# Performance work log

Measured on AMD Instinct MI355X. Metric: run time of the kernel, lower is better.

The kernel has to match this reference:

```python
import jax, jax.numpy as jnp
import numpy as np

T, B, D_IN = 1024, 64, 17
H_MAIN = 150   # per-direction hidden of main bi-GRU (hidden_dim=300)
H_HIER = 128   # per-direction hidden of hier bi-GRU (hier_hidden=256)
M = 16         # uniform measure length (eoM fires every M steps)
N_MEAS = T // M
N_PITCH, N_KS = 35, 15
PAD_P, PAD_K = 34, 14


def _gru(x, Wih, Whh, bih, bhh):
    # x: [T, N, D]; torch GRU gate order is (r, z, n)
    H = Whh.shape[1]
    gi_all = jnp.einsum('tnd,gd->tng', x, Wih) + bih  # input-side gates, precomputed

    def step(h, gi):
        gh = h @ Whh.T + bhh
        ir, iz, inn = jnp.split(gi, 3, axis=-1)
        hr, hz, hn = jnp.split(gh, 3, axis=-1)
        r = jax.nn.sigmoid(ir + hr)
        z = jax.nn.sigmoid(iz + hz)
        n = jnp.tanh(inn + r * hn)
        h_new = (1.0 - z) * n + z * h
        return h_new, h_new

    h0 = jnp.zeros((x.shape[1], H), x.dtype)
    _, ys = jax.lax.scan(step, h0, gi_all)
    return ys


def _bigru(x, pf, pb):
    yf = _gru(x, *pf)
    yb = _gru(x[::-1], *pb)[::-1]
    return jnp.concatenate([yf, yb], axis=-1)


def _ce(logits, targets, pad_idx):
    # mean cross-entropy with ignore_index=pad_idx
    logp = jax.nn.log_softmax(logits, axis=-1)
    mask = (targets != pad_idx).astype(logits.dtype)
    nll = -jnp.take_along_axis(logp, targets[:, None], axis=1)[:, 0]
    return jnp.sum(nll * mask) / jnp.maximum(jnp.sum(mask), 1.0)


def _forward(sentences, mWih_f, mWhh_f, mbih_f, mbhh_f, mWih_b, mWhh_b, mbih_b, mbhh_b,
             hWih_f, hWhh_f, hbih_f, hbhh_f, hWih_b, hWhh_b, hbih_b, hbhh_b,
             Wq, bq, Wv, bv, Wp, bp, Wk, bk, pitches, keysignatures):
    # main bi-GRU over full sequences: [T, B, 300]
    rnn_out = _bigru(sentences, (mWih_f, mWhh_f, mbih_f, mbhh_f),
                     (mWih_b, mWhh_b, mbih_b, mbhh_b))
    H2 = rnn_out.shape[-1]
    # carve uniform measures: [T,B,H2] -> [M, B*N_MEAS, H2]
    seg = rnn_out.reshape(N_MEAS, M, B, H2).transpose(1, 2, 0, 3).reshape(M, B * N_MEAS, H2)
    hier = _bigru(seg, (hWih_f, hWhh_f, hbih_f, hbhh_f),
                  (hWih_b, hWhh_b, hbih_b, hbhh_b))  # [M, B*N_MEAS, 256]
    HH = hier.shape[-1]
    # attention per measure: query = value = hier outputs [B*N_MEAS, M, 256]
    hv = hier.reshape(M, B, N_MEAS, HH).transpose(1, 2, 0, 3).reshape(B * N_MEAS, M, HH)
    q = hv @ Wq.T + bq
    v = hv @ Wv.T + bv
    attn = jax.nn.softmax(jnp.einsum('nld,nmd->nlm', q, v), axis=-1)
    ctx = jnp.einsum('nlm,nmd->nd', attn, hv).reshape(B, N_MEAS, HH)  # sum over l of attn@value
    # repeat each measure context over its M timesteps: [T, B, 256]
    ctx_t = jnp.repeat(ctx, M, axis=1).transpose(1, 0, 2)
    stacked = jnp.concatenate([rnn_out, ctx_t], axis=-1)  # [T, B, 556]
    out_pitch = stacked @ Wp.T + bp   # [T, B, 35]
    out_ks = ctx_t @ Wk.T + bk        # [T, B, 15]
    return (_ce(out_pitch.reshape(-1, N_PITCH), pitches.reshape(-1), PAD_P)
            + _ce(out_ks.reshape(-1, N_KS), keysignatures.reshape(-1), PAD_K))


def setup_inputs() -> dict:
    key = jax.random.key(0)
    ks = jax.random.split(key, 32)

    def w(i, *shape):
        return jax.random.normal(ks[i], shape, jnp.float32) * 0.05

    G_M, G_H = 3 * H_MAIN, 3 * H_HIER
    inp = {
        'sentences': jax.random.normal(ks[0], (T, B, D_IN), jnp.float32),
        'pitches': jax.random.randint(ks[1], (T, B), 0, PAD_P),
        'keysignatures': jax.random.randint(ks[2], (T, B), 0, PAD_K),
        'sentences_len': jnp.full((B,), T, dtype=jnp.int32),
        'eoM': jnp.tile(((jnp.arange(T) % M) == M - 1).astype(jnp.int32)[:, None], (1, B)),
        'mWih_f': w(3, G_M, D_IN), 'mWhh_f': w(4, G_M, H_MAIN), 'mbih_f': w(5, G_M), 'mbhh_f': w(6, G_M),
        'mWih_b': w(7, G_M, D_IN), 'mWhh_b': w(8, G_M, H_MAIN), 'mbih_b': w(9, G_M), 'mbhh_b': w(10, G_M),
        'hWih_f': w(11, G_H, 2 * H_MAIN), 'hWhh_f': w(12, G_H, H_HIER), 'hbih_f': w(13, G_H), 'hbhh_f': w(14, G_H),
        'hWih_b': w(15, G_H, 2 * H_MAIN), 'hWhh_b': w(16, G_H, H_HIER), 'hbih_b': w(17, G_H), 'hbhh_b': w(18, G_H),
        'Wq': w(19, 2 * H_HIER, 2 * H_HIER), 'bq': w(20, 2 * H_HIER),
        'Wv': w(21, 2 * H_HIER, 2 * H_HIER), 'bv': w(22, 2 * H_HIER),
        'Wp': w(23, N_PITCH, 2 * H_MAIN + 2 * H_HIER), 'bp': w(24, N_PITCH),
        'Wk': w(25, N_KS, 2 * H_HIER), 'bk': w(26, N_KS),
    }
    return inp


def reference(sentences, pitches, keysignatures, sentences_len, eoM,
              mWih_f, mWhh_f, mbih_f, mbhh_f, mWih_b, mWhh_b, mbih_b, mbhh_b,
              hWih_f, hWhh_f, hbih_f, hbhh_f, hWih_b, hWhh_b, hbih_b, hbhh_b,
              Wq, bq, Wv, bv, Wp, bp, Wk, bk):
    # sentences_len/eoM encode the (uniform) measure structure M=16, full lengths;
    # the segment layout is baked in statically, so they are structural constants here.
    return _forward(sentences, mWih_f, mWhh_f, mbih_f, mbhh_f, mWih_b, mWhh_b, mbih_b, mbhh_b,
                    hWih_f, hWhh_f, hbih_f, hbhh_f, hWih_b, hWhh_b, hbih_b, hbhh_b,
                    Wq, bq, Wv, bv, Wp, bp, Wk, bk, pitches, keysignatures)
```

## Files before the change

### kernel.cpp

```cpp
#include <hip/hip_runtime.h>
#include <cstddef>

constexpr int kT   = 1024;
constexpr int kB   = 64;
constexpr int kDIN = 17;
constexpr int kHM  = 150;
constexpr int kHH  = 128;
constexpr int kM   = 16;
constexpr int kD2  = 300;
constexpr int kNP  = 35;
constexpr int kNK  = 15;

constexpr size_t OFF_RNN16  = 0;
constexpr size_t OFF_HV16   = 10485760;
constexpr size_t OFF_CTX    = 18874368;
constexpr size_t OFF_PT     = 19922944;
constexpr size_t OFF_PTPACK = 19988480;
constexpr size_t OFF_U      = 20021248;
constexpr size_t OFF_W      = 20021504;
constexpr size_t OFF_C0     = 20021760;
constexpr size_t OFF_ACC    = 20021776;
constexpr size_t OFF_KSLOGP = 20021792;
constexpr size_t OFF_CLOG   = 20083232;
constexpr size_t OFF_BPACKM = 20226592;
constexpr size_t OFF_BPACK  = 20318752;
constexpr size_t OFF_BPACKL = 20490784;

typedef __bf16 bf16x8 __attribute__((ext_vector_type(8)));
typedef float f32x4 __attribute__((ext_vector_type(4)));

__device__ __forceinline__ unsigned short f2bf(float f) {
  unsigned u = __float_as_uint(f);
  u += 0x7FFFu + ((u >> 16) & 1u);
  return (unsigned short)(u >> 16);
}
__device__ __forceinline__ float bf2f(unsigned short v) {
  return __uint_as_float(((unsigned)v) << 16);
}
__device__ __forceinline__ float sigm(float x) {
  return __builtin_amdgcn_rcpf(1.f + __expf(-x));
}
__device__ __forceinline__ float tanh_fast(float x) {
  return 1.f - 2.f * __builtin_amdgcn_rcpf(__expf(2.f * x) + 1.f);
}

__global__ void k_pt(const float* __restrict__ Wq, const float* __restrict__ Wv,
                     float* __restrict__ PT) {
  const int e = blockIdx.x, c = threadIdx.x;
  float acc = 0.f;
  for (int a = 0; a < 256; a++) acc += Wq[a * 256 + c] * Wv[a * 256 + e];
  PT[e * 256 + c] = acc;
}

__global__ void k_ptsmall(const float* __restrict__ PT,
                          const float* __restrict__ Wq, const float* __restrict__ bq,
                          const float* __restrict__ Wv, const float* __restrict__ bv,
                          unsigned short* __restrict__ pp,
                          float* __restrict__ u, float* __restrict__ w,
                          float* __restrict__ c0, float* __restrict__ acc) {
  const int bid = blockIdx.x;
  if (bid < 128) {
    if (threadIdx.x >= 64) return;
    const int kt = bid & 7, nt = bid >> 3;
    const int lane = threadIdx.x;
    const int c = nt * 16 + (lane & 15);
    const int e0 = kt * 32 + (lane >> 4) * 8;
#pragma unroll
    for (int j = 0; j < 8; j++)
      pp[((size_t)bid * 64 + lane) * 8 + j] = f2bf(PT[(e0 + j) * 256 + c]);
  } else {
    const int a = threadIdx.x;
    float us = 0.f, ws = 0.f;
    for (int j = 0; j < 256; j++) {
      us += Wq[j * 256 + a] * bv[j];
      ws += bq[j] * Wv[j * 256 + a];
    }
    u[a] = us; w[a] = ws;
    if (a == 0) {
      float c = 0.f;
      for (int j = 0; j < 256; j++) c += bq[j] * bv[j];
      c0[0] = c;
      acc[0] = acc[1] = acc[2] = acc[3] = 0.f;
    }
  }
}

__global__ void k_repack_all(
    const float* __restrict__ mWih_f, const float* __restrict__ mWhh_f,
    const float* __restrict__ mWih_b, const float* __restrict__ mWhh_b,
    const float* __restrict__ hWih_f, const float* __restrict__ hWhh_f,
    const float* __restrict__ hWih_b, const float* __restrict__ hWhh_b,
    const float* __restrict__ Wp,
    unsigned short* __restrict__ bpackM, unsigned short* __restrict__ bpack,
    unsigned short* __restrict__ bpackL) {
  const int lane = threadIdx.x;
  int bid = blockIdx.x;
  if (bid < 360) {
    const int kt = bid % 6;
    const int gt = (bid / 6) % 30;
    const int d  = bid / 180;
    const float* Wih = d ? mWih_b : mWih_f;
    const float* Whh = d ? mWhh_b : mWhh_f;
    const int slot = gt * 16 + (lane & 15);
    const int type = slot / 160, j = slot - type * 160;
    const int row = type * 150 + j;
    const bool valid = (j < 150);
    const int kbase = (lane >> 4) * 8;
    unsigned short* dst = bpackM + ((((size_t)d * 30 + gt) * 6 + kt) * 64 + lane) * 8;
#pragma unroll
    for (int jj = 0; jj < 8; jj++) {
      float f = 0.f;
      if (valid) {
        if (kt < 5) {
          const int k = kt * 32 + kbase + jj;
          if (k < 150) f = Whh[row * 150 + k];
        } else {
          const int k = kbase + jj;
          if (k < 17) f = Wih[row * 17 + k];
        }
      }
      dst[jj] = f2bf(f);
    }
  } else if (bid < 1032) {
    bid -= 360;
    const int kt = bid % 14;
    const int nt = (bid / 14) % 24;
    const int d  = bid / (14 * 24);
    const float* Wih = d ? hWih_b : hWih_f;
    const float* Whh = d ? hWhh_b : hWhh_f;
    const int n = nt * 16 + (lane & 15);
    const int kbase = kt * 32 + (lane >> 4) * 8;
    unsigned short* dst = bpack + ((((size_t)d * 24 + nt) * 14 + kt) * 64 + lane) * 8;
#pragma unroll
    for (int j = 0; j < 8; j++) {
      const int k = kbase + j;
      float f = 0.f;
      if (kt < 10) {
        if (k < 150) f = Wih[n * 300 + k];
        else if (k >= 160 && k < 310) f = Wih[n * 300 + (k - 10)];
      } else {
        f = Whh[n * 128 + (k - 320)];
      }
      dst[j] = f2bf(f);
    }
  } else {
    bid -= 1032;
    const int kt = bid % 10, nt = bid / 10;
    const int n = nt * 16 + (lane & 15);
    const int kbase = kt * 32 + (lane >> 4) * 8;
    unsigned short* dst = bpackL + (((size_t)bid) * 64 + lane) * 8;
#pragma unroll
    for (int j = 0; j < 8; j++) {
      const int k = kbase + j;
      float f = 0.f;
      if (n < kNP) {
        if (k < 150) f = Wp[n * 556 + k];
        else if (k >= 160 && k < 310) f = Wp[n * 556 + (k - 10)];
      }
      dst[j] = f2bf(f);
    }
  }
}

__global__ __launch_bounds__(640, 2) void k_main_gru_mfma(
    const float* __restrict__ x,
    const unsigned short* __restrict__ bpackM,
    const float* __restrict__ bihf, const float* __restrict__ bhhf,
    const float* __restrict__ bihb, const float* __restrict__ bhhb,
    unsigned short* __restrict__ rnn16)
{
  const int d = blockIdx.x & 1, b = blockIdx.x >> 1;
  const int tid = threadIdx.x, w = tid >> 6, lane = tid & 63;
  const int col = lane & 15, q8 = (lane >> 4) * 8;
  __shared__ __align__(16) unsigned short hx[2][160];
  __shared__ __align__(16) unsigned short hist[2][16][160];
  __shared__ __align__(16) unsigned short xall[kT][32];
  for (int i = tid; i < 2 * 160; i += 640) ((unsigned short*)hx)[i] = 0;
  for (int i = tid; i < 2 * 16 * 160; i += 640) ((unsigned short*)hist)[i] = 0;
  for (int i = tid; i < kT * 32; i += 640) {
    const int t = i >> 5, c = i & 31;
    xall[t][c] = (c < kDIN) ? f2bf(x[((size_t)t * kB + b) * kDIN + c]) : (unsigned short)0;
  }
  const float* bih = d ? bihb : bihf;
  const float* bhh = d ? bhhb : bhhf;
  const int j = w * 16 + col;
  const bool actv = (lane < 16) && (j < kHM);
  float br = 0.f, bz = 0.f, bnx = 0.f, bnh = 0.f;
  if (actv) {
    br  = bih[j] + bhh[j];
    bz  = bih[150 + j] + bhh[150 + j];
    bnx = bih[300 + j];
    bnh = bhh[300 + j];
  }
  bf16x8 bw[3][6];
  const unsigned short* bp = bpackM + (size_t)d * 30 * 6 * 64 * 8;
  const int gts[3] = { w, 10 + w, 20 + w };
#pragma unroll
  for (int gi = 0; gi < 3; gi++)
#pragma unroll
    for (int kt = 0; kt < 6; kt++)
      bw[gi][kt] = *(const bf16x8*)&bp[(((size_t)gts[gi] * 6 + kt) * 64 + lane) * 8];
  float h_old = 0.f;
  __syncthreads();

  for (int t = 0; t < kT; t++) {
    const int tx = d ? (kT - 1 - t) : t;
    const int buf = t & 1;
    bf16x8 afr[6];
#pragma unroll
    for (int kt = 0; kt < 5; kt++) afr[kt] = *(const bf16x8*)&hx[buf][kt * 32 + q8];
    afr[5] = *(const bf16x8*)&xall[tx][q8];
    f32x4 aR0 = (f32x4)(0.f), aR1 = (f32x4)(0.f);
    f32x4 aZ0 = (f32x4)(0.f), aZ1 = (f32x4)(0.f);
    f32x4 aN0 = (f32x4)(0.f), aN1 = (f32x4)(0.f);
    f32x4 aX  = (f32x4)(0.f);
#pragma unroll
    for (int kt = 0; kt < 6; kt++) {
      const bf16x8 af = afr[kt];
      if ((kt & 1) == 0) {
        aR0 = __builtin_amdgcn_mfma_f32_16x16x32_bf16(af, bw[0][kt], aR0, 0, 0, 0);
        aZ0 = __builtin_amdgcn_mfma_f32_16x16x32_bf16(af, bw[1][kt], aZ0, 0, 0, 0);
        aN0 = __builtin_amdgcn_mfma_f32_16x16x32_bf16(af, bw[2][kt], aN0, 0, 0, 0);
      } else if (kt < 5) {
        aR1 = __builtin_amdgcn_mfma_f32_16x16x32_bf16(af, bw[0][kt], aR1, 0, 0, 0);
        aZ1 = __builtin_amdgcn_mfma_f32_16x16x32_bf16(af, bw[1][kt], aZ1, 0, 0, 0);
        aN1 = __builtin_amdgcn_mfma_f32_16x16x32_bf16(af, bw[2][kt], aN1, 0, 0, 0);
      } else {
        aR1 = __builtin_amdgcn_mfma_f32_16x16x32_bf16(af, bw[0][5], aR1, 0, 0, 0);
        aZ1 = __builtin_amdgcn_mfma_f32_16x16x32_bf16(af, bw[1][5], aZ1, 0, 0, 0);
        aX  = __builtin_amdgcn_mfma_f32_16x16x32_bf16(af, bw[2][5], aX, 0, 0, 0);
      }
    }
    if (actv) {
      const float r = sigm(aR0[0] + aR1[0] + br);
      const float z = sigm(aZ0[0] + aZ1[0] + bz);
      const float n = tanh_fast(aX[0] + bnx + r * (aN0[0] + aN1[0] + bnh));
      h_old = (1.f - z) * n + z * h_old;
      const unsigned short us = f2bf(h_old);
      hx[buf ^ 1][j] = us;
      hist[(t >> 4) & 1][t & 15][j] = us;
    }
    __syncthreads();
    if ((t & 15) == 15) {
      const int hb = (t >> 4) & 1;
      const int toff = tid / 40, ch = tid - toff * 40;
      const int tg = t - 15 + toff;
      const int txg = d ? (kT - 1 - tg) : tg;
      *(ushort4*)&rnn16[((size_t)txg * kB + b) * 320 + d * 160 + ch * 4] =
          *(const ushort4*)&hist[hb][toff][ch * 4];
    }
  }
}

__global__ __launch_bounds__(512, 1) void k_hier_mfma(
    const unsigned short* __restrict__ rnn16,
    const unsigned short* __restrict__ bpack,
    const float* __restrict__ bihf, const float* __restrict__ bhhf,
    const float* __restrict__ bihb, const float* __restrict__ bhhb,
    unsigned short* __restrict__ hv16)
{
  const int d = blockIdx.x & 1;
  const int bn0 = (blockIdx.x >> 1) * 16;
  const int tid = threadIdx.x;
  const int w = tid >> 6;
  const int lane = tid & 63;
  const int q = lane >> 4, col = lane & 15, q8 = q * 8;

  __shared__ __align__(16) unsigned short x_s[2][16][328];
  __shared__ __align__(16) unsigned short h_s[16][136];

  for (int i = tid; i < 16 * 136; i += 512) ((unsigned short*)h_s)[i] = 0;
  const float* bih = d ? bihb : bihf;
  const float* bhh = d ? bhhb : bhhf;
  const int j = w * 16 + col;
  const float biR  = bih[j] + bhh[j];
  const float biZ  = bih[128 + j] + bhh[128 + j];
  const float biNX = bih[256 + j];
  const float biNH = bhh[256 + j];
  float h32r[4] = {0.f, 0.f, 0.f, 0.f};

  bf16x8 bw[3][14];
  const unsigned short* bpd = bpack + (size_t)d * 24 * 14 * 64 * 8;
  const int nts[3] = { w, 8 + w, 16 + w };
#pragma unroll
  for (int gi = 0; gi < 3; gi++)
#pragma unroll
    for (int kt = 0; kt < 14; kt++)
      bw[gi][kt] = *(const bf16x8*)&bpd[(((size_t)nts[gi] * 14 + kt) * 64 + lane) * 8];

  {
    const int mx0 = d ? 15 : 0;
    for (int i = tid; i < 640; i += 512) {
      const int r = i / 40, c = i - r * 40;
      const int bn = bn0 + r, bb = bn >> 6, nn = bn & 63;
      *(uint4*)&x_s[0][r][c * 8] =
          *(const uint4*)&rnn16[((size_t)(nn * 16 + mx0) * 64 + bb) * 320 + c * 8];
    }
  }
  __syncthreads();

  for (int m = 0; m < kM; m++) {
    const int mx = d ? (15 - m) : m;
    const int buf = m & 1;
    f32x4 aR = (f32x4)(0.f), aZ = (f32x4)(0.f), aNX = (f32x4)(0.f), aNH = (f32x4)(0.f);
#pragma unroll
    for (int kt = 0; kt < 14; kt++) {
      const bf16x8 af = (kt < 10) ? *(const bf16x8*)&x_s[buf][col][kt * 32 + q8]
                                  : *(const bf16x8*)&h_s[col][(kt - 10) * 32 + q8];
      aR = __builtin_amdgcn_mfma_f32_16x16x32_bf16(af, bw[0][kt], aR, 0, 0, 0);
      aZ = __builtin_amdgcn_mfma_f32_16x16x32_bf16(af, bw[1][kt], aZ, 0, 0, 0);
      if (kt < 10) aNX = __builtin_amdgcn_mfma_f32_16x16x32_bf16(af, bw[2][kt], aNX, 0, 0, 0);
      else         aNH = __builtin_amdgcn_mfma_f32_16x16x32_bf16(af, bw[2][kt], aNH, 0, 0, 0);
    }
    __syncthreads();
#pragma unroll
    for (int i = 0; i < 4; i++) {
      const int row = q * 4 + i;
      const float rr = sigm(aR[i] + biR);
      const float zz = sigm(aZ[i] + biZ);
      const float nn2 = tanh_fast(aNX[i] + biNX + rr * (aNH[i] + biNH));
      const float hnew = (1.f - zz) * nn2 + zz * h32r[i];
      h32r[i] = hnew;
      const unsigned short us = f2bf(hnew);
      h_s[row][j] = us;
      hv16[((size_t)(bn0 + row) * kM + mx) * 256 + d * kHH + j] = us;
    }
    if (m + 1 < kM) {
      const int mxn = d ? (15 - (m + 1)) : (m + 1);
      for (int i = tid; i < 640; i += 512) {
        const int r = i / 40, c = i - r * 40;
        const int bn = bn0 + r, bb = bn >> 6, nn = bn & 63;
        *(uint4*)&x_s[buf ^ 1][r][c * 8] =
            *(const uint4*)&rnn16[((size_t)(nn * 16 + mxn) * 64 + bb) * 320 + c * 8];
      }
    }
    __syncthreads();
  }
}

__global__ __launch_bounds__(256) void k_attn2(
    const unsigned short* __restrict__ hv16, const unsigned short* __restrict__ ptpack,
    const float* __restrict__ u, const float* __restrict__ w,
    const float* __restrict__ c0p, float* __restrict__ ctx) {
  const int tid = threadIdx.x;
  const int wv = tid >> 6, lane = tid & 63, col = lane & 15, q = lane >> 4, q8 = q * 8;
  __shared__ __align__(16) unsigned short hv16s[16][264];
  __shared__ __align__(16) unsigned short Ts16[16][264];
  __shared__ float pu[16][17], pw[16][17];
  __shared__ float uh[16], wh[16], SM[16];
  __shared__ float As[16][17];
  const float c0 = c0p[0];
  bf16x8 bpt[4][8];
#pragma unroll
  for (int i2 = 0; i2 < 4; i2++)
#pragma unroll
    for (int kt = 0; kt < 8; kt++)
      bpt[i2][kt] = *(const bf16x8*)&ptpack[((((size_t)(wv * 4 + i2)) * 8 + kt) * 64 + lane) * 8];

  for (int ni = 0; ni < 4; ni++) {
    const int n = blockIdx.x * 4 + ni;
    {
      const unsigned short* src = hv16 + (size_t)n * 4096;
      const int row = tid >> 4, ci = (tid & 15) * 16;
#pragma unroll
      for (int k = 0; k < 16; k += 4)
        *(ushort4*)&hv16s[row][ci + k] = *(const ushort4*)&src[row * 256 + ci + k];
    }
    __syncthreads();
    {
      f32x4 acc[4];
#pragma unroll
      for (int i2 = 0; i2 < 4; i2++) acc[i2] = (f32x4)(0.f);
#pragma unroll
      for (int kt = 0; kt < 8; kt++) {
        const bf16x8 af = *(const bf16x8*)&hv16s[col][kt * 32 + q8];
#pragma unroll
        for (int i2 = 0; i2 < 4; i2++)
          acc[i2] = __builtin_amdgcn_mfma_f32_16x16x32_bf16(af, bpt[i2][kt], acc[i2], 0, 0, 0);
      }
#pragma unroll
      for (int i2 = 0; i2 < 4; i2++) {
        const int nt = wv * 4 + i2;
#pragma unroll
        for (int i = 0; i < 4; i++) Ts16[q * 4 + i][nt * 16 + col] = f2bf(acc[i2][i]);
      }
    }
    {
      const int l = tid >> 4, s = tid & 15;
      float su = 0.f, sw = 0.f;
#pragma unroll
      for (int a0 = 0; a0 < 16; a0++) {
        const int a = s * 16 + a0;
        const float hvv = bf2f(hv16s[l][a]);
        su += hvv * u[a];
        sw += hvv * w[a];
      }
      pu[l][s] = su; pw[l][s] = sw;
    }
    __syncthreads();
    if (tid < 16) { float s2 = 0.f; for (int s = 0; s < 16; s++) s2 += pu[tid][s]; uh[tid] = s2; }
    else if (tid < 32) { float s2 = 0.f; for (int s = 0; s < 16; s++) s2 += pw[tid - 16][s]; wh[tid - 16] = s2; }
    __syncthreads();
    if (tid < 64) {
      f32x4 sa = (f32x4)(0.f);
#pragma unroll
      for (int kt = 0; kt < 8; kt++) {
        const bf16x8 af  = *(const bf16x8*)&hv16s[col][kt * 32 + q8];
        const bf16x8 bts = *(const bf16x8*)&Ts16[col][kt * 32 + q8];
        sa = __builtin_amdgcn_mfma_f32_16x16x32_bf16(af, bts, sa, 0, 0, 0);
      }
#pragma unroll
      for (int i = 0; i < 4; i++) {
        const int l = q * 4 + i;
        float sc = sa[i] + c0 + uh[l] + wh[col];
        float mxv = sc;
#pragma unroll
        for (int o = 8; o >= 1; o >>= 1) mxv = fmaxf(mxv, __shfl_xor(mxv, o, 16));
        const float e = __expf(sc - mxv);
        float se = e;
#pragma unroll
        for (int o = 8; o >= 1; o >>= 1) se += __shfl_xor(se, o, 16);
        As[l][col] = e / se;
      }
    }
    __syncthreads();
    if (tid < 16) {
      float s = 0.f;
      for (int l2 = 0; l2 < 16; l2++) s += As[l2][tid];
      SM[tid] = s;
    }
    __syncthreads();
    float cv = 0.f;
#pragma unroll
    for (int m2 = 0; m2 < 16; m2++) cv += SM[m2] * bf2f(hv16s[m2][tid]);
    ctx[(size_t)n * 256 + tid] = cv;
    __syncthreads();
  }
}

__global__ __launch_bounds__(256) void k_ctxlog2(
    const float* __restrict__ ctx, const float* __restrict__ Wp, const float* __restrict__ bp,
    const float* __restrict__ Wk, const float* __restrict__ bk,
    float* __restrict__ clog, float* __restrict__ kslogp) {
  const int tid = threadIdx.x;
  __shared__ __align__(16) float W2[50][260];
  __shared__ __align__(16) float cs[256];
  __shared__ float arr[64];
  __shared__ float bps[35], bks[15];
  for (int i = tid; i < 35 * 256; i += 256) { const int r = i >> 8, c = i & 255; W2[r][c] = Wp[r * 556 + 300 + c]; }
  for (int i = tid; i < 15 * 256; i += 256) { const int r = i >> 8, c = i & 255; W2[35 + r][c] = Wk[r * 256 + c]; }
  if (tid < 35) bps[tid] = bp[tid];
  else if (tid < 50) bks[tid - 35] = bk[tid - 35];
  __syncthreads();
  const int o = tid >> 2, s = tid & 3;
  for (int it = 0; it < 16; it++) {
    const int bn = blockIdx.x * 16 + it;
    cs[tid] = ctx[(size_t)bn * 256 + tid];
    __syncthreads();
    float v = 0.f;
    if (o < 50) {
      for (int k0 = 0; k0 < 64; k0 += 4) {
        const int k = s * 64 + k0;
        const float4 wq = *(const float4*)&W2[o][k];
        const float4 cq = *(const float4*)&cs[k];
        v += wq.x * cq.x + wq.y * cq.y + wq.z * cq.z + wq.w * cq.w;
      }
    }
    v += __shfl_xor(v, 1);
    v += __shfl_xor(v, 2);
    if (o < 50 && s == 0) arr[o] = v;
    __syncthreads();
    if (tid < 35) clog[bn * kNP + tid] = arr[tid] + bps[tid];
    if (tid >= 64 && tid < 80) {
      const int t2 = tid - 64;
      float kk = (t2 < 15) ? arr[35 + t2] + bks[t2] : -1e30f;
      float mxv = kk;
#pragma unroll
      for (int off = 8; off >= 1; off >>= 1) mxv = fmaxf(mxv, __shfl_xor(mxv, off, 16));
      const float e = (t2 < 15) ? __expf(kk - mxv) : 0.f;
      float se = e;
#pragma unroll
      for (int off = 8; off >= 1; off >>= 1) se += __shfl_xor(se, off, 16);
      if (t2 < 15) kslogp[bn * kNK + t2] = kk - mxv - __logf(se);
    }
    __syncthreads();
  }
}

__global__ __launch_bounds__(256, 2) void k_loss_mfma(
    const unsigned short* __restrict__ rnn16,
    const unsigned short* __restrict__ bpackL,
    const float* __restrict__ clog,
    const float* __restrict__ ks_logp,
    const int* __restrict__ pitches, const int* __restrict__ kss,
    float* __restrict__ acc) {
  const int tid = threadIdx.x, w = tid >> 6, lane = tid & 63;
  const int col = lane & 15, q = lane >> 4, q8 = q * 8;
  bf16x8 bl[3][10];
#pragma unroll
  for (int nt = 0; nt < 3; nt++)
#pragma unroll
    for (int kt = 0; kt < 10; kt++)
      bl[nt][kt] = *(const bf16x8*)&bpackL[(((size_t)nt * 10 + kt) * 64 + lane) * 8];

  float sp = 0.f, cp = 0.f, sk = 0.f, ck = 0.f;
#pragma unroll
  for (int mt = 0; mt < 2; mt++) {
    const int rowbase = blockIdx.x * 128 + w * 32 + mt * 16;
    f32x4 a0 = (f32x4)(0.f), a1 = (f32x4)(0.f), a2 = (f32x4)(0.f);
#pragma unroll
    for (int kt = 0; kt < 10; kt++) {
      const bf16x8 af = *(const bf16x8*)&rnn16[(size_t)(rowbase + col) * 320 + kt * 32 + q8];
      a0 = __builtin_amdgcn_mfma_f32_16x16x32_bf16(af, bl[0][kt], a0, 0, 0, 0);
      a1 = __builtin_amdgcn_mfma_f32_16x16x32_bf16(af, bl[1][kt], a1, 0, 0, 0);
      a2 = __builtin_amdgcn_mfma_f32_16x16x32_bf16(af, bl[2][kt], a2, 0, 0, 0);
    }
#pragma unroll
    for (int i = 0; i < 4; i++) {
      const int row = rowbase + q * 4 + i;
      const int t = row >> 6, b = row & 63;
      const int bn = b * 64 + (t >> 4);
      const float lg0 = a0[i] + clog[bn * kNP + col];
      const float lg1 = a1[i] + clog[bn * kNP + 16 + col];
      const float lg2 = (col < 3) ? (a2[i] + clog[bn * kNP + 32 + col]) : -1e30f;
      float mx = fmaxf(fmaxf(lg0, lg1), lg2);
#pragma unroll
      for (int o = 8; o >= 1; o >>= 1) mx = fmaxf(mx, __shfl_xor(mx, o, 16));
      float se = __expf(lg0 - mx) + __expf(lg1 - mx) + __expf(lg2 - mx);
#pragma unroll
      for (int o = 8; o >= 1; o >>= 1) se += __shfl_xor(se, o, 16);
      const int tp = pitches[row];
      const float cand = (tp < 16) ? a0[i] : (tp < 32) ? a1[i] : a2[i];
      const float tva = __shfl(cand, (lane & 48) | (tp & 15), 64);
      if (col == 0 && tp != 34) {
        sp += (mx + __logf(se)) - (tva + clog[bn * kNP + tp]);
        cp += 1.f;
      }
      if (col == 1) {
        const int tk = kss[row];
        if (tk != 14) { sk -= ks_logp[bn * kNK + tk]; ck += 1.f; }
      }
    }
  }
#pragma unroll
  for (int o = 32; o >= 1; o >>= 1) {
    sp += __shfl_xor(sp, o, 64);
    cp += __shfl_xor(cp, o, 64);
    sk += __shfl_xor(sk, o, 64);
    ck += __shfl_xor(ck, o, 64);
  }
  if (lane == 0) {
    atomicAdd(&acc[0], sp); atomicAdd(&acc[1], cp);
    atomicAdd(&acc[2], sk); atomicAdd(&acc[3], ck);
  }
}

__global__ void k_final(const float* __restrict__ acc, float* __restrict__ out) {
  out[0] = acc[0] / fmaxf(acc[1], 1.f) + acc[2] / fmaxf(acc[3], 1.f);
}

extern "C" void kernel_launch(void* const* d_in, const int* in_sizes, int n_in,
                              void* d_out, int out_size, void* d_ws, size_t ws_size,
                              hipStream_t stream) {
  (void)in_sizes; (void)n_in; (void)out_size; (void)ws_size;
  const float* sent    = (const float*)d_in[0];
  const int*   pitches = (const int*)d_in[1];
  const int*   kss     = (const int*)d_in[2];
  const float* mWih_f  = (const float*)d_in[5];
  const float* mWhh_f  = (const float*)d_in[6];
  const float* mbih_f  = (const float*)d_in[7];
  const float* mbhh_f  = (const float*)d_in[8];
  const float* mWih_b  = (const float*)d_in[9];
  const float* mWhh_b  = (const float*)d_in[10];
  const float* mbih_b  = (const float*)d_in[11];
  const float* mbhh_b  = (const float*)d_in[12];
  const float* hWih_f  = (const float*)d_in[13];
  const float* hWhh_f  = (const float*)d_in[14];
  const float* hbih_f  = (const float*)d_in[15];
  const float* hbhh_f  = (const float*)d_in[16];
  const float* hWih_b  = (const float*)d_in[17];
  const float* hWhh_b  = (const float*)d_in[18];
  const float* hbih_b  = (const float*)d_in[19];
  const float* hbhh_b  = (const float*)d_in[20];
  const float* Wq      = (const float*)d_in[21];
  const float* bq      = (const float*)d_in[22];
  const float* Wv      = (const float*)d_in[23];
  const float* bv      = (const float*)d_in[24];
  const float* Wp      = (const float*)d_in[25];
  const float* bp      = (const float*)d_in[26];
  const float* Wk      = (const float*)d_in[27];
  const float* bk      = (const float*)d_in[28];
  float* ws  = (float*)d_ws;
  float* out = (float*)d_out;
  unsigned short* rnn16  = (unsigned short*)(ws + OFF_RNN16);
  unsigned short* hv16   = (unsigned short*)(ws + OFF_HV16);
  unsigned short* ptpack = (unsigned short*)(ws + OFF_PTPACK);
  unsigned short* bpackL = (unsigned short*)(ws + OFF_BPACKL);

  k_repack_all<<<1062, 64, 0, stream>>>(mWih_f, mWhh_f, mWih_b, mWhh_b,
                                        hWih_f, hWhh_f, hWih_b, hWhh_b, Wp,
                                        (unsigned short*)(ws + OFF_BPACKM),
                                        (unsigned short*)(ws + OFF_BPACK), bpackL);
  k_pt<<<256, 256, 0, stream>>>(Wq, Wv, ws + OFF_PT);
  k_ptsmall<<<129, 256, 0, stream>>>(ws + OFF_PT, Wq, bq, Wv, bv, ptpack,
                                     ws + OFF_U, ws + OFF_W, ws + OFF_C0, ws + OFF_ACC);

  k_main_gru_mfma<<<128, 640, 0, stream>>>(sent, (const unsigned short*)(ws + OFF_BPACKM),
                                           mbih_f, mbhh_f, mbih_b, mbhh_b, rnn16);
  k_hier_mfma<<<512, 512, 0, stream>>>(rnn16, (const unsigned short*)(ws + OFF_BPACK),
                                       hbih_f, hbhh_f, hbih_b, hbhh_b, hv16);
  k_attn2<<<1024, 256, 0, stream>>>(hv16, ptpack, ws + OFF_U, ws + OFF_W,
                                    ws + OFF_C0, ws + OFF_CTX);
  k_ctxlog2<<<256, 256, 0, stream>>>(ws + OFF_CTX, Wp, bp, Wk, bk,
                                     ws + OFF_CLOG, ws + OFF_KSLOGP);
  k_loss_mfma<<<512, 256, 0, stream>>>(rnn16, bpackL, ws + OFF_CLOG, ws + OFF_KSLOGP,
                                       pitches, kss, ws + OFF_ACC);
  k_final<<<1, 1, 0, stream>>>(ws + OFF_ACC, out);
}
```

Baseline: 1.047 ms.

## Fold weight prep into main GRU mega-kernel and fuse attention with context logits

The three prologue kernels (repack, PT product, small vectors) are merged into one launch with the main bi-GRU. The main GRU blocks now load and convert their recurrent weights directly from fp32 instead of reading a pre-packed buffer, and the remaining prep work runs on spare blocks in parallel with the serial recurrence. Attention and the context-to-logits projection are fused so the ctx buffer round-trip and one launch disappear, with each block now handling 16 measures instead of 4. This cuts launch count and serial prologue latency, at the cost of fewer attention blocks (256 instead of 1024) and slower per-thread weight loading inside the GRU blocks.

```diff
diff --git a/kernel.cpp b/kernel.cpp
--- a/kernel.cpp
+++ b/kernel.cpp
@@ -13,8 +13,6 @@
 
 constexpr size_t OFF_RNN16  = 0;
 constexpr size_t OFF_HV16   = 10485760;
-constexpr size_t OFF_CTX    = 18874368;
-constexpr size_t OFF_PT     = 19922944;
 constexpr size_t OFF_PTPACK = 19988480;
 constexpr size_t OFF_U      = 20021248;
 constexpr size_t OFF_W      = 20021504;
@@ -22,7 +20,6 @@
 constexpr size_t OFF_ACC    = 20021776;
 constexpr size_t OFF_KSLOGP = 20021792;
 constexpr size_t OFF_CLOG   = 20083232;
-constexpr size_t OFF_BPACKM = 20226592;
 constexpr size_t OFF_BPACK  = 20318752;
 constexpr size_t OFF_BPACKL = 20490784;
 
@@ -44,210 +41,203 @@
   return 1.f - 2.f * __builtin_amdgcn_rcpf(__expf(2.f * x) + 1.f);
 }
 
-__global__ void k_pt(const float* __restrict__ Wq, const float* __restrict__ Wv,
-                     float* __restrict__ PT) {
-  const int e = blockIdx.x, c = threadIdx.x;
-  float acc = 0.f;
-  for (int a = 0; a < 256; a++) acc += Wq[a * 256 + c] * Wv[a * 256 + e];
-  PT[e * 256 + c] = acc;
-}
-
-__global__ void k_ptsmall(const float* __restrict__ PT,
-                          const float* __restrict__ Wq, const float* __restrict__ bq,
-                          const float* __restrict__ Wv, const float* __restrict__ bv,
-                          unsigned short* __restrict__ pp,
-                          float* __restrict__ u, float* __restrict__ w,
-                          float* __restrict__ c0, float* __restrict__ acc) {
-  const int bid = blockIdx.x;
-  if (bid < 128) {
-    if (threadIdx.x >= 64) return;
-    const int kt = bid & 7, nt = bid >> 3;
-    const int lane = threadIdx.x;
-    const int c = nt * 16 + (lane & 15);
-    const int e0 = kt * 32 + (lane >> 4) * 8;
-#pragma unroll
-    for (int j = 0; j < 8; j++)
-      pp[((size_t)bid * 64 + lane) * 8 + j] = f2bf(PT[(e0 + j) * 256 + c]);
-  } else {
-    const int a = threadIdx.x;
-    float us = 0.f, ws = 0.f;
-    for (int j = 0; j < 256; j++) {
-      us += Wq[j * 256 + a] * bv[j];
-      ws += bq[j] * Wv[j * 256 + a];
-    }
-    u[a] = us; w[a] = ws;
-    if (a == 0) {
-      float c = 0.f;
-      for (int j = 0; j < 256; j++) c += bq[j] * bv[j];
-      c0[0] = c;
-      acc[0] = acc[1] = acc[2] = acc[3] = 0.f;
-    }
-  }
-}
-
-__global__ void k_repack_all(
+__global__ __launch_bounds__(640, 2) void k_mega(
+    const float* __restrict__ x,
     const float* __restrict__ mWih_f, const float* __restrict__ mWhh_f,
     const float* __restrict__ mWih_b, const float* __restrict__ mWhh_b,
+    const float* __restrict__ mbih_f, const float* __restrict__ mbhh_f,
+    const float* __restrict__ mbih_b, const float* __restrict__ mbhh_b,
     const float* __restrict__ hWih_f, const float* __restrict__ hWhh_f,
     const float* __restrict__ hWih_b, const float* __restrict__ hWhh_b,
     const float* __restrict__ Wp,
-    unsigned short* __restrict__ bpackM, unsigned short* __restrict__ bpack,
-    unsigned short* __restrict__ bpackL) {
-  const int lane = threadIdx.x;
-  int bid = blockIdx.x;
-  if (bid < 360) {
-    const int kt = bid % 6;
-    const int gt = (bid / 6) % 30;
-    const int d  = bid / 180;
-    const float* Wih = d ? mWih_b : mWih_f;
-    const float* Whh = d ? mWhh_b : mWhh_f;
-    const int slot = gt * 16 + (lane & 15);
-    const int type = slot / 160, j = slot - type * 160;
-    const int row = type * 150 + j;
-    const bool valid = (j < 150);
-    const int kbase = (lane >> 4) * 8;
-    unsigned short* dst = bpackM + ((((size_t)d * 30 + gt) * 6 + kt) * 64 + lane) * 8;
-#pragma unroll
-    for (int jj = 0; jj < 8; jj++) {
-      float f = 0.f;
-      if (valid) {
-        if (kt < 5) {
-          const int k = kt * 32 + kbase + jj;
-          if (k < 150) f = Whh[row * 150 + k];
-        } else {
-          const int k = kbase + jj;
-          if (k < 17) f = Wih[row * 17 + k];
-        }
-      }
-      dst[jj] = f2bf(f);
-    }
-  } else if (bid < 1032) {
-    bid -= 360;
-    const int kt = bid % 14;
-    const int nt = (bid / 14) % 24;
-    const int d  = bid / (14 * 24);
-    const float* Wih = d ? hWih_b : hWih_f;
-    const float* Whh = d ? hWhh_b : hWhh_f;
-    const int n = nt * 16 + (lane & 15);
-    const int kbase = kt * 32 + (lane >> 4) * 8;
-    unsigned short* dst = bpack + ((((size_t)d * 24 + nt) * 14 + kt) * 64 + lane) * 8;
-#pragma unroll
-    for (int j = 0; j < 8; j++) {
-      const int k = kbase + j;
-      float f = 0.f;
-      if (kt < 10) {
-        if (k < 150) f = Wih[n * 300 + k];
-        else if (k >= 160 && k < 310) f = Wih[n * 300 + (k - 10)];
-      } else {
-        f = Whh[n * 128 + (k - 320)];
-      }
-      dst[j] = f2bf(f);
-    }
-  } else {
-    bid -= 1032;
-    const int kt = bid % 10, nt = bid / 10;
-    const int n = nt * 16 + (lane & 15);
-    const int kbase = kt * 32 + (lane >> 4) * 8;
-    unsigned short* dst = bpackL + (((size_t)bid) * 64 + lane) * 8;
-#pragma unroll
-    for (int j = 0; j < 8; j++) {
-      const int k = kbase + j;
-      float f = 0.f;
-      if (n < kNP) {
-        if (k < 150) f = Wp[n * 556 + k];
-        else if (k >= 160 && k < 310) f = Wp[n * 556 + (k - 10)];
-      }
-      dst[j] = f2bf(f);
-    }
-  }
-}
-
-__global__ __launch_bounds__(640, 2) void k_main_gru_mfma(
-    const float* __restrict__ x,
-    const unsigned short* __restrict__ bpackM,
-    const float* __restrict__ bihf, const float* __restrict__ bhhf,
-    const float* __restrict__ bihb, const float* __restrict__ bhhb,
-    unsigned short* __restrict__ rnn16)
+    const float* __restrict__ Wq, const float* __restrict__ bq,
+    const float* __restrict__ Wv, const float* __restrict__ bv,
+    unsigned short* __restrict__ rnn16,
+    unsigned short* __restrict__ bpack,
+    unsigned short* __restrict__ bpackL,
+    unsigned short* __restrict__ pp,
+    float* __restrict__ u, float* __restrict__ w,
+    float* __restrict__ c0, float* __restrict__ acc)
 {
-  const int d = blockIdx.x & 1, b = blockIdx.x >> 1;
-  const int tid = threadIdx.x, w = tid >> 6, lane = tid & 63;
-  const int col = lane & 15, q8 = (lane >> 4) * 8;
   __shared__ __align__(16) unsigned short hx[2][160];
   __shared__ __align__(16) unsigned short hist[2][16][160];
   __shared__ __align__(16) unsigned short xall[kT][32];
-  for (int i = tid; i < 2 * 160; i += 640) ((unsigned short*)hx)[i] = 0;
-  for (int i = tid; i < 2 * 16 * 160; i += 640) ((unsigned short*)hist)[i] = 0;
-  for (int i = tid; i < kT * 32; i += 640) {
-    const int t = i >> 5, c = i & 31;
-    xall[t][c] = (c < kDIN) ? f2bf(x[((size_t)t * kB + b) * kDIN + c]) : (unsigned short)0;
-  }
-  const float* bih = d ? bihb : bihf;
-  const float* bhh = d ? bhhb : bhhf;
-  const int j = w * 16 + col;
-  const bool actv = (lane < 16) && (j < kHM);
-  float br = 0.f, bz = 0.f, bnx = 0.f, bnh = 0.f;
-  if (actv) {
-    br  = bih[j] + bhh[j];
-    bz  = bih[150 + j] + bhh[150 + j];
-    bnx = bih[300 + j];
-    bnh = bhh[300 + j];
-  }
-  bf16x8 bw[3][6];
-  const unsigned short* bp = bpackM + (size_t)d * 30 * 6 * 64 * 8;
-  const int gts[3] = { w, 10 + w, 20 + w };
-#pragma unroll
-  for (int gi = 0; gi < 3; gi++)
-#pragma unroll
-    for (int kt = 0; kt < 6; kt++)
-      bw[gi][kt] = *(const bf16x8*)&bp[(((size_t)gts[gi] * 6 + kt) * 64 + lane) * 8];
-  float h_old = 0.f;
-  __syncthreads();
-
-  for (int t = 0; t < kT; t++) {
-    const int tx = d ? (kT - 1 - t) : t;
-    const int buf = t & 1;
-    bf16x8 afr[6];
-#pragma unroll
-    for (int kt = 0; kt < 5; kt++) afr[kt] = *(const bf16x8*)&hx[buf][kt * 32 + q8];
-    afr[5] = *(const bf16x8*)&xall[tx][q8];
-    f32x4 aR0 = (f32x4)(0.f), aR1 = (f32x4)(0.f);
-    f32x4 aZ0 = (f32x4)(0.f), aZ1 = (f32x4)(0.f);
-    f32x4 aN0 = (f32x4)(0.f), aN1 = (f32x4)(0.f);
-    f32x4 aX  = (f32x4)(0.f);
-#pragma unroll
-    for (int kt = 0; kt < 6; kt++) {
-      const bf16x8 af = afr[kt];
-      if ((kt & 1) == 0) {
-        aR0 = __builtin_amdgcn_mfma_f32_16x16x32_bf16(af, bw[0][kt], aR0, 0, 0, 0);
-        aZ0 = __builtin_amdgcn_mfma_f32_16x16x32_bf16(af, bw[1][kt], aZ0, 0, 0, 0);
-        aN0 = __builtin_amdgcn_mfma_f32_16x16x32_bf16(af, bw[2][kt], aN0, 0, 0, 0);
-      } else if (kt < 5) {
-        aR1 = __builtin_amdgcn_mfma_f32_16x16x32_bf16(af, bw[0][kt], aR1, 0, 0, 0);
-        aZ1 = __builtin_amdgcn_mfma_f32_16x16x32_bf16(af, bw[1][kt], aZ1, 0, 0, 0);
-        aN1 = __builtin_amdgcn_mfma_f32_16x16x32_bf16(af, bw[2][kt], aN1, 0, 0, 0);
-      } else {
-        aR1 = __builtin_amdgcn_mfma_f32_16x16x32_bf16(af, bw[0][5], aR1, 0, 0, 0);
-        aZ1 = __builtin_amdgcn_mfma_f32_16x16x32_bf16(af, bw[1][5], aZ1, 0, 0, 0);
-        aX  = __builtin_amdgcn_mfma_f32_16x16x32_bf16(af, bw[2][5], aX, 0, 0, 0);
-      }
-    }
+  const int blk = blockIdx.x;
+  if (blk < 128) {
+    const int d = blk & 1, b = blk >> 1;
+    const int tid = threadIdx.x, wv = tid >> 6, lane = tid & 63;
+    const int col = lane & 15, q8 = (lane >> 4) * 8;
+    for (int i = tid; i < 2 * 160; i += 640) ((unsigned short*)hx)[i] = 0;
+    for (int i = tid; i < 2 * 16 * 160; i += 640) ((unsigned short*)hist)[i] = 0;
+    for (int i = tid; i < kT * 32; i += 640) {
+      const int t = i >> 5, c = i & 31;
+      xall[t][c] = (c < kDIN) ? f2bf(x[((size_t)t * kB + b) * kDIN + c]) : (unsigned short)0;
+    }
+    const float* bih = d ? mbih_b : mbih_f;
+    const float* bhh = d ? mbhh_b : mbhh_f;
+    const float* Wihd = d ? mWih_b : mWih_f;
+    const float* Whhd = d ? mWhh_b : mWhh_f;
+    const int j = wv * 16 + col;
+    const bool actv = (lane < 16) && (j < kHM);
+    float br = 0.f, bz = 0.f, bnx = 0.f, bnh = 0.f;
     if (actv) {
-      const float r = sigm(aR0[0] + aR1[0] + br);
-      const float z = sigm(aZ0[0] + aZ1[0] + bz);
-      const float n = tanh_fast(aX[0] + bnx + r * (aN0[0] + aN1[0] + bnh));
-      h_old = (1.f - z) * n + z * h_old;
-      const unsigned short us = f2bf(h_old);
-      hx[buf ^ 1][j] = us;
-      hist[(t >> 4) & 1][t & 15][j] = us;
-    }
-    __syncthreads();
-    if ((t & 15) == 15) {
-      const int hb = (t >> 4) & 1;
-      const int toff = tid / 40, ch = tid - toff * 40;
-      const int tg = t - 15 + toff;
-      const int txg = d ? (kT - 1 - tg) : tg;
-      *(ushort4*)&rnn16[((size_t)txg * kB + b) * 320 + d * 160 + ch * 4] =
-          *(const ushort4*)&hist[hb][toff][ch * 4];
+      br  = bih[j] + bhh[j];
+      bz  = bih[150 + j] + bhh[150 + j];
+      bnx = bih[300 + j];
+      bnh = bhh[300 + j];
+    }
+    bf16x8 bw[3][6];
+    const int gts[3] = { wv, 10 + wv, 20 + wv };
+#pragma unroll
+    for (int gi = 0; gi < 3; gi++) {
+      const int slot = gts[gi] * 16 + col;
+      const int type = slot / 160, jh = slot - type * 160;
+      const int row = type * 150 + jh;
+      const bool valid = (jh < 150);
+#pragma unroll
+      for (int kt = 0; kt < 6; kt++) {
+        union { bf16x8 v; unsigned short us[8]; } tmp;
+#pragma unroll
+        for (int jj = 0; jj < 8; jj++) {
+          float f = 0.f;
+          if (valid) {
+            if (kt < 5) {
+              const int k = kt * 32 + (lane >> 4) * 8 + jj;
+              if (k < 150) f = Whhd[row * 150 + k];
+            } else {
+              const int k = (lane >> 4) * 8 + jj;
+              if (k < 17) f = Wihd[row * 17 + k];
+            }
+          }
+          tmp.us[jj] = f2bf(f);
+        }
+        bw[gi][kt] = tmp.v;
+      }
+    }
+    float h_old = 0.f;
+    __syncthreads();
+
+    for (int t = 0; t < kT; t++) {
+      const int tx = d ? (kT - 1 - t) : t;
+      const int buf = t & 1;
+      bf16x8 afr[6];
+#pragma unroll
+      for (int kt = 0; kt < 5; kt++) afr[kt] = *(const bf16x8*)&hx[buf][kt * 32 + q8];
+      afr[5] = *(const bf16x8*)&xall[tx][q8];
+      f32x4 aR0 = (f32x4)(0.f), aR1 = (f32x4)(0.f);
+      f32x4 aZ0 = (f32x4)(0.f), aZ1 = (f32x4)(0.f);
+      f32x4 aN0 = (f32x4)(0.f), aN1 = (f32x4)(0.f);
+      f32x4 aX  = (f32x4)(0.f);
+#pragma unroll
+      for (int kt = 0; kt < 6; kt++) {
+        const bf16x8 af = afr[kt];
+        if ((kt & 1) == 0) {
+          aR0 = __builtin_amdgcn_mfma_f32_16x16x32_bf16(af, bw[0][kt], aR0, 0, 0, 0);
+          aZ0 = __builtin_amdgcn_mfma_f32_16x16x32_bf16(af, bw[1][kt], aZ0, 0, 0, 0);
+          aN0 = __builtin_amdgcn_mfma_f32_16x16x32_bf16(af, bw[2][kt], aN0, 0, 0, 0);
+        } else if (kt < 5) {
+          aR1 = __builtin_amdgcn_mfma_f32_16x16x32_bf16(af, bw[0][kt], aR1, 0, 0, 0);
+          aZ1 = __builtin_amdgcn_mfma_f32_16x16x32_bf16(af, bw[1][kt], aZ1, 0, 0, 0);
+          aN1 = __builtin_amdgcn_mfma_f32_16x16x32_bf16(af, bw[2][kt], aN1, 0, 0, 0);
+        } else {
+          aR1 = __builtin_amdgcn_mfma_f32_16x16x32_bf16(af, bw[0][5], aR1, 0, 0, 0);
+          aZ1 = __builtin_amdgcn_mfma_f32_16x16x32_bf16(af, bw[1][5], aZ1, 0, 0, 0);
+          aX  = __builtin_amdgcn_mfma_f32_16x16x32_bf16(af, bw[2][5], aX, 0, 0, 0);
+        }
+      }
+      if (actv) {
+        const float r = sigm(aR0[0] + aR1[0] + br);
+        const float z = sigm(aZ0[0] + aZ1[0] + bz);
+        const float n = tanh_fast(aX[0] + bnx + r * (aN0[0] + aN1[0] + bnh));
+        h_old = (1.f - z) * n + z * h_old;
+        const unsigned short us = f2bf(h_old);
+        hx[buf ^ 1][j] = us;
+        hist[(t >> 4) & 1][t & 15][j] = us;
+      }
+      __syncthreads();
+      if ((t & 15) == 15) {
+        const int hb = (t >> 4) & 1;
+        const int toff = tid / 40, ch = tid - toff * 40;
+        const int tg = t - 15 + toff;
+        const int txg = d ? (kT - 1 - tg) : tg;
+        *(ushort4*)&rnn16[((size_t)txg * kB + b) * 320 + d * 160 + ch * 4] =
+            *(const ushort4*)&hist[hb][toff][ch * 4];
+      }
+    }
+  } else if (blk < 199) {
+    const int sub = threadIdx.x >> 6, lane = threadIdx.x & 63;
+    int bid = (blk - 128) * 10 + sub;
+    if (bid >= 702) return;
+    if (bid < 672) {
+      const int kt = bid % 14;
+      const int nt = (bid / 14) % 24;
+      const int d  = bid / (14 * 24);
+      const float* Wih = d ? hWih_b : hWih_f;
+      const float* Whh = d ? hWhh_b : hWhh_f;
+      const int n = nt * 16 + (lane & 15);
+      const int kbase = kt * 32 + (lane >> 4) * 8;
+      unsigned short* dst = bpack + ((((size_t)d * 24 + nt) * 14 + kt) * 64 + lane) * 8;
+#pragma unroll
+      for (int jj = 0; jj < 8; jj++) {
+        const int k = kbase + jj;
+        float f = 0.f;
+        if (kt < 10) {
+          if (k < 150) f = Wih[n * 300 + k];
+          else if (k >= 160 && k < 310) f = Wih[n * 300 + (k - 10)];
+        } else {
+          f = Whh[n * 128 + (k - 320)];
+        }
+        dst[jj] = f2bf(f);
+      }
+    } else {
+      bid -= 672;
+      const int kt = bid % 10, nt = bid / 10;
+      const int n = nt * 16 + (lane & 15);
+      const int kbase = kt * 32 + (lane >> 4) * 8;
+      unsigned short* dst = bpackL + (((size_t)bid) * 64 + lane) * 8;
+#pragma unroll
+      for (int jj = 0; jj < 8; jj++) {
+        const int k = kbase + jj;
+        float f = 0.f;
+        if (n < kNP) {
+          if (k < 150) f = Wp[n * 556 + k];
+          else if (k >= 160 && k < 310) f = Wp[n * 556 + (k - 10)];
+        }
+        dst[jj] = f2bf(f);
+      }
+    }
+  } else if (blk < 212) {
+    const int sub = threadIdx.x >> 6, lane = threadIdx.x & 63;
+    const int bid = (blk - 199) * 10 + sub;
+    if (bid >= 128) return;
+    const int kt = bid & 7, nt = bid >> 3;
+    const int c = nt * 16 + (lane & 15);
+    const int e0 = kt * 32 + (lane >> 4) * 8;
+    float av[8];
+#pragma unroll
+    for (int jj = 0; jj < 8; jj++) av[jj] = 0.f;
+    for (int a = 0; a < 256; a++) {
+      const float wq = Wq[a * 256 + c];
+#pragma unroll
+      for (int jj = 0; jj < 8; jj++) av[jj] += wq * Wv[a * 256 + e0 + jj];
+    }
+    unsigned short* dst = pp + ((size_t)bid * 64 + lane) * 8;
+#pragma unroll
+    for (int jj = 0; jj < 8; jj++) dst[jj] = f2bf(av[jj]);
+  } else {
+    const int a = threadIdx.x;
+    if (a >= 256) return;
+    float us = 0.f, ws = 0.f;
+    for (int jj = 0; jj < 256; jj++) {
+      us += Wq[jj * 256 + a] * bv[jj];
+      ws += bq[jj] * Wv[jj * 256 + a];
+    }
+    u[a] = us; w[a] = ws;
+    if (a == 0) {
+      float cc = 0.f;
+      for (int jj = 0; jj < 256; jj++) cc += bq[jj] * bv[jj];
+      c0[0] = cc;
+      acc[0] = acc[1] = acc[2] = acc[3] = 0.f;
     }
   }
 }
@@ -338,18 +328,29 @@
   }
 }
 
-__global__ __launch_bounds__(256) void k_attn2(
+__global__ __launch_bounds__(256) void k_attn_ctx(
     const unsigned short* __restrict__ hv16, const unsigned short* __restrict__ ptpack,
     const float* __restrict__ u, const float* __restrict__ w,
-    const float* __restrict__ c0p, float* __restrict__ ctx) {
+    const float* __restrict__ c0p,
+    const float* __restrict__ Wp, const float* __restrict__ bp,
+    const float* __restrict__ Wk, const float* __restrict__ bk,
+    float* __restrict__ clog, float* __restrict__ kslogp) {
   const int tid = threadIdx.x;
   const int wv = tid >> 6, lane = tid & 63, col = lane & 15, q = lane >> 4, q8 = q * 8;
   __shared__ __align__(16) unsigned short hv16s[16][264];
   __shared__ __align__(16) unsigned short Ts16[16][264];
+  __shared__ __align__(16) float W2[50][260];
+  __shared__ __align__(16) float cs[256];
   __shared__ float pu[16][17], pw[16][17];
   __shared__ float uh[16], wh[16], SM[16];
   __shared__ float As[16][17];
+  __shared__ float arr[64];
+  __shared__ float bps[35], bks[15];
   const float c0 = c0p[0];
+  for (int i = tid; i < 35 * 256; i += 256) { const int r = i >> 8, c = i & 255; W2[r][c] = Wp[r * 556 + 300 + c]; }
+  for (int i = tid; i < 15 * 256; i += 256) { const int r = i >> 8, c = i & 255; W2[35 + r][c] = Wk[r * 256 + c]; }
+  if (tid < 35) bps[tid] = bp[tid];
+  else if (tid < 50) bks[tid - 35] = bk[tid - 35];
   bf16x8 bpt[4][8];
 #pragma unroll
   for (int i2 = 0; i2 < 4; i2++)
@@ -357,8 +358,8 @@
     for (int kt = 0; kt < 8; kt++)
       bpt[i2][kt] = *(const bf16x8*)&ptpack[((((size_t)(wv * 4 + i2)) * 8 + kt) * 64 + lane) * 8];
 
-  for (int ni = 0; ni < 4; ni++) {
-    const int n = blockIdx.x * 4 + ni;
+  for (int ni = 0; ni < 16; ni++) {
+    const int n = blockIdx.x * 16 + ni;
     {
       const unsigned short* src = hv16 + (size_t)n * 4096;
       const int row = tid >> 4, ci = (tid & 15) * 16;
@@ -368,21 +369,21 @@
     }
     __syncthreads();
     {
-      f32x4 acc[4];
-#pragma unroll
-      for (int i2 = 0; i2 < 4; i2++) acc[i2] = (f32x4)(0.f);
+      f32x4 acc4[4];
+#pragma unroll
+      for (int i2 = 0; i2 < 4; i2++) acc4[i2] = (f32x4)(0.f);
 #pragma unroll
       for (int kt = 0; kt < 8; kt++) {
         const bf16x8 af = *(const bf16x8*)&hv16s[col][kt * 32 + q8];
 #pragma unroll
         for (int i2 = 0; i2 < 4; i2++)
-          acc[i2] = __builtin_amdgcn_mfma_f32_16x16x32_bf16(af, bpt[i2][kt], acc[i2], 0, 0, 0);
+          acc4[i2] = __builtin_amdgcn_mfma_f32_16x16x32_bf16(af, bpt[i2][kt], acc4[i2], 0, 0, 0);
       }
 #pragma unroll
       for (int i2 = 0; i2 < 4; i2++) {
         const int nt = wv * 4 + i2;
 #pragma unroll
-        for (int i = 0; i < 4; i++) Ts16[q * 4 + i][nt * 16 + col] = f2bf(acc[i2][i]);
+        for (int i = 0; i < 4; i++) Ts16[q * 4 + i][nt * 16 + col] = f2bf(acc4[i2][i]);
       }
     }
     {
@@ -430,47 +431,30 @@
       SM[tid] = s;
     }
     __syncthreads();
-    float cv = 0.f;
-#pragma unroll
-    for (int m2 = 0; m2 < 16; m2++) cv += SM[m2] * bf2f(hv16s[m2][tid]);
-    ctx[(size_t)n * 256 + tid] = cv;
-    __syncthreads();
-  }
-}
-
-__global__ __launch_bounds__(256) void k_ctxlog2(
-    const float* __restrict__ ctx, const float* __restrict__ Wp, const float* __restrict__ bp,
-    const float* __restrict__ Wk, const float* __restrict__ bk,
-    float* __restrict__ clog, float* __restrict__ kslogp) {
-  const int tid = threadIdx.x;
-  __shared__ __align__(16) float W2[50][260];
-  __shared__ __align__(16) float cs[256];
-  __shared__ float arr[64];
-  __shared__ float bps[35], bks[15];
-  for (int i = tid; i < 35 * 256; i += 256) { const int r = i >> 8, c = i & 255; W2[r][c] = Wp[r * 556 + 300 + c]; }
-  for (int i = tid; i < 15 * 256; i += 256) { const int r = i >> 8, c = i & 255; W2[35 + r][c] = Wk[r * 256 + c]; }
-  if (tid < 35) bps[tid] = bp[tid];
-  else if (tid < 50) bks[tid - 35] = bk[tid - 35];
-  __syncthreads();
-  const int o = tid >> 2, s = tid & 3;
-  for (int it = 0; it < 16; it++) {
-    const int bn = blockIdx.x * 16 + it;
-    cs[tid] = ctx[(size_t)bn * 256 + tid];
-    __syncthreads();
-    float v = 0.f;
-    if (o < 50) {
-      for (int k0 = 0; k0 < 64; k0 += 4) {
-        const int k = s * 64 + k0;
-        const float4 wq = *(const float4*)&W2[o][k];
-        const float4 cq = *(const float4*)&cs[k];
-        v += wq.x * cq.x + wq.y * cq.y + wq.z * cq.z + wq.w * cq.w;
-      }
-    }
-    v += __shfl_xor(v, 1);
-    v += __shfl_xor(v, 2);
-    if (o < 50 && s == 0) arr[o] = v;
-    __syncthreads();
-    if (tid < 35) clog[bn * kNP + tid] = arr[tid] + bps[tid];
+    {
+      float cv = 0.f;
+#pragma unroll
+      for (int m2 = 0; m2 < 16; m2++) cv += SM[m2] * bf2f(hv16s[m2][tid]);
+      cs[tid] = cv;
+    }
+    __syncthreads();
+    {
+      const int o = tid >> 2, s = tid & 3;
+      float v = 0.f;
+      if (o < 50) {
+        for (int k0 = 0; k0 < 64; k0 += 4) {
+          const int k = s * 64 + k0;
+          const float4 wq = *(const float4*)&W2[o][k];
+          const float4 cq = *(const float4*)&cs[k];
+          v += wq.x * cq.x + wq.y * cq.y + wq.z * cq.z + wq.w * cq.w;
+        }
+      }
+      v += __shfl_xor(v, 1);
+      v += __shfl_xor(v, 2);
+      if (o < 50 && s == 0) arr[o] = v;
+    }
+    __syncthreads();
+    if (tid < 35) clog[n * kNP + tid] = arr[tid] + bps[tid];
     if (tid >= 64 && tid < 80) {
       const int t2 = tid - 64;
       float kk = (t2 < 15) ? arr[35 + t2] + bks[t2] : -1e30f;
@@ -481,7 +465,7 @@
       float se = e;
 #pragma unroll
       for (int off = 8; off >= 1; off >>= 1) se += __shfl_xor(se, off, 16);
-      if (t2 < 15) kslogp[bn * kNK + t2] = kk - mxv - __logf(se);
+      if (t2 < 15) kslogp[n * kNK + t2] = kk - mxv - __logf(se);
     }
     __syncthreads();
   }
@@ -596,23 +580,20 @@
   unsigned short* hv16   = (unsigned short*)(ws + OFF_HV16);
   unsigned short* ptpack = (unsigned short*)(ws + OFF_PTPACK);
   unsigned short* bpackL = (unsigned short*)(ws + OFF_BPACKL);
-
-  k_repack_all<<<1062, 64, 0, stream>>>(mWih_f, mWhh_f, mWih_b, mWhh_b,
-                                        hWih_f, hWhh_f, hWih_b, hWhh_b, Wp,
-                                        (unsigned short*)(ws + OFF_BPACKM),
-                                        (unsigned short*)(ws + OFF_BPACK), bpackL);
-  k_pt<<<256, 256, 0, stream>>>(Wq, Wv, ws + OFF_PT);
-  k_ptsmall<<<129, 256, 0, stream>>>(ws + OFF_PT, Wq, bq, Wv, bv, ptpack,
-                                     ws + OFF_U, ws + OFF_W, ws + OFF_C0, ws + OFF_ACC);
-
-  k_main_gru_mfma<<<128, 640, 0, stream>>>(sent, (const unsigned short*)(ws + OFF_BPACKM),
-                                           mbih_f, mbhh_f, mbih_b, mbhh_b, rnn16);
-  k_hier_mfma<<<512, 512, 0, stream>>>(rnn16, (const unsigned short*)(ws + OFF_BPACK),
+  unsigned short* bpack  = (unsigned short*)(ws + OFF_BPACK);
+
+  k_mega<<<213, 640, 0, stream>>>(sent,
+                                  mWih_f, mWhh_f, mWih_b, mWhh_b,
+                                  mbih_f, mbhh_f, mbih_b, mbhh_b,
+                                  hWih_f, hWhh_f, hWih_b, hWhh_b, Wp,
+                                  Wq, bq, Wv, bv,
+                                  rnn16, bpack, bpackL, ptpack,
+                                  ws + OFF_U, ws + OFF_W, ws + OFF_C0, ws + OFF_ACC);
+  k_hier_mfma<<<512, 512, 0, stream>>>(rnn16, bpack,
                                        hbih_f, hbhh_f, hbih_b, hbhh_b, hv16);
-  k_attn2<<<1024, 256, 0, stream>>>(hv16, ptpack, ws + OFF_U, ws + OFF_W,
-                                    ws + OFF_C0, ws + OFF_CTX);
-  k_ctxlog2<<<256, 256, 0, stream>>>(ws + OFF_CTX, Wp, bp, Wk, bk,
-                                     ws + OFF_CLOG, ws + OFF_KSLOGP);
+  k_attn_ctx<<<256, 256, 0, stream>>>(hv16, ptpack, ws + OFF_U, ws + OFF_W,
+                                      ws + OFF_C0, Wp, bp, Wk, bk,
+                                      ws + OFF_CLOG, ws + OFF_KSLOGP);
   k_loss_mfma<<<512, 256, 0, stream>>>(rnn16, bpackL, ws + OFF_CLOG, ws + OFF_KSLOGP,
                                        pitches, kss, ws + OFF_ACC);
   k_final<<<1, 1, 0, stream>>>(ws + OFF_ACC, out);
```

Measured after the change: 1.042 ms. About the same (-0.5%).
